# Kernel tuning notes

Measured on AMD Instinct MI355X. Metric: run time of the kernel, lower is better.

Reference implementation:

```python
import jax, jax.numpy as jnp
import numpy as np

N_QUBITS = 4
N_LAYERS = 2


def _ry(theta):
    # PennyLane RY(theta) = [[cos(t/2), -sin(t/2)], [sin(t/2), cos(t/2)]]
    c = jnp.cos(theta / 2)
    s = jnp.sin(theta / 2)
    return jnp.stack([jnp.stack([c, -s]), jnp.stack([s, c])]).astype(jnp.complex64)


def _rz(theta):
    # PennyLane RZ(theta) = diag(exp(-i t/2), exp(+i t/2))
    e = jnp.exp(-0.5j * theta.astype(jnp.complex64))
    return jnp.diag(jnp.stack([e, jnp.conj(e)]))


def _apply_1q(state, U, wire):
    # state: (2,)*N_QUBITS complex; contract U into axis `wire`
    state = jnp.tensordot(U, state, axes=((1,), (wire,)))
    return jnp.moveaxis(state, 0, wire)


def _cnot(state, ctrl, tgt):
    s = jnp.moveaxis(state, ctrl, 0)
    t2 = tgt - 1 if tgt > ctrl else tgt
    s1 = jnp.flip(s[1], axis=t2)  # X on target where control == 1
    return jnp.moveaxis(jnp.stack([s[0], s1]), 0, ctrl)


def _circuit(angles, weights):
    # angles: (N_QUBITS,), weights: (N_LAYERS, N_QUBITS, 2)
    state = jnp.zeros((2,) * N_QUBITS, jnp.complex64).at[(0,) * N_QUBITS].set(1.0)
    for i in range(N_QUBITS):
        state = _apply_1q(state, _ry(angles[i]), i)
    for l in range(N_LAYERS):
        for i in range(N_QUBITS):
            state = _apply_1q(state, _ry(weights[l, i, 0]), i)
            state = _apply_1q(state, _rz(weights[l, i, 1]), i)
        for i in range(N_QUBITS - 1):
            state = _cnot(state, i, i + 1)
        state = _cnot(state, N_QUBITS - 1, 0)
    probs = jnp.abs(state) ** 2
    p = probs.reshape(2, -1).sum(axis=1)  # marginal on wire 0
    return p[0] - p[1]  # <Z_0>


def setup_inputs() -> dict:
    key = jax.random.key(0)
    ks = jax.random.split(key, 6)
    B = 65536
    return {
        "x": jax.random.normal(ks[0], (B, 256), jnp.float32),
        "W1": jax.random.normal(ks[1], (64, 256), jnp.float32) * 0.0625,
        "b1": jax.random.normal(ks[2], (64,), jnp.float32) * 0.01,
        "W2": jax.random.normal(ks[3], (4, 64), jnp.float32) * 0.125,
        "b2": jax.random.normal(ks[4], (4,), jnp.float32) * 0.01,
        "q_weights": jax.random.normal(ks[5], (N_LAYERS, N_QUBITS, 2), jnp.float32) * 0.1,
    }


def reference(x, W1, b1, W2, b2, q_weights):
    h = jax.nn.relu(x @ W1.T + b1)          # [B, 64]
    angles = jnp.tanh(h @ W2.T + b2)         # [B, 4]
    z = jax.vmap(lambda a: _circuit(a, q_weights))(angles)  # [B]
    return z[:, None]                        # [B, 1]
```

## Files before the change

### kernel.cpp

```cpp
#include <hip/hip_runtime.h>
#include <math.h>

#define BM   64
#define BK   64
#define KDIM 256
#define LDSW 68
#define HSW  65

__global__ __launch_bounds__(256, 4)
void qc_fused(const float* __restrict__ x,
              const float* __restrict__ W1,
              const float* __restrict__ b1,
              const float* __restrict__ W2,
              const float* __restrict__ b2,
              const float* __restrict__ qw,
              float* __restrict__ out)
{
    __shared__ float smem[2 * BK * LDSW];
    __shared__ float w2s[4 * 64];
    __shared__ float b1s[64];
    __shared__ float b2s[4];
    __shared__ float trig[2 * 4 * 4];

    float (*xs)[LDSW] = (float(*)[LDSW])smem;
    float (*ws)[LDSW] = (float(*)[LDSW])(smem + BK * LDSW);

    const int tid  = threadIdx.x;
    const int tx   = tid & 15;
    const int ty   = tid >> 4;
    const int row0 = blockIdx.x * BM;

    w2s[tid] = W2[tid];
    if (tid < 64) b1s[tid] = b1[tid];
    if (tid < 4)  b2s[tid] = b2[tid];
    if (tid < 8) {
        int l = tid >> 2, i = tid & 3;
        float wy = qw[(l * 4 + i) * 2 + 0];
        float wz = qw[(l * 4 + i) * 2 + 1];
        float sy, cy, sz, cz;
        sincosf(0.5f * wy, &sy, &cy);
        sincosf(0.5f * wz, &sz, &cz);
        trig[(l * 4 + i) * 4 + 0] = cy;
        trig[(l * 4 + i) * 4 + 1] = sy;
        trig[(l * 4 + i) * 4 + 2] = cz;
        trig[(l * 4 + i) * 4 + 3] = sz;
    }

    float acc[4][4] = {};

    const int lr = tid >> 4;
    const int kq = tid & 15;

    for (int kt = 0; kt < KDIM / BK; ++kt) {
        if (kt) __syncthreads();
        #pragma unroll
        for (int rr = 0; rr < 4; ++rr) {
            int r = rr * 16 + lr;
            float4 xv = *(const float4*)(x  + (size_t)(row0 + r) * KDIM + kt * BK + kq * 4);
            float4 wv = *(const float4*)(W1 + (size_t)r          * KDIM + kt * BK + kq * 4);
            xs[kq * 4 + 0][r] = xv.x; xs[kq * 4 + 1][r] = xv.y;
            xs[kq * 4 + 2][r] = xv.z; xs[kq * 4 + 3][r] = xv.w;
            ws[kq * 4 + 0][r] = wv.x; ws[kq * 4 + 1][r] = wv.y;
            ws[kq * 4 + 2][r] = wv.z; ws[kq * 4 + 3][r] = wv.w;
        }
        __syncthreads();
        #pragma unroll 8
        for (int k = 0; k < BK; ++k) {
            float4 xa = *(const float4*)&xs[k][4 * ty];
            float4 wa = *(const float4*)&ws[k][4 * tx];
            float xr[4] = {xa.x, xa.y, xa.z, xa.w};
            float wc[4] = {wa.x, wa.y, wa.z, wa.w};
            #pragma unroll
            for (int i = 0; i < 4; ++i)
                #pragma unroll
                for (int j = 0; j < 4; ++j)
                    acc[i][j] = fmaf(xr[i], wc[j], acc[i][j]);
        }
    }
    __syncthreads();

    float* hsf = smem;
    #pragma unroll
    for (int i = 0; i < 4; ++i)
        #pragma unroll
        for (int j = 0; j < 4; ++j) {
            float v = acc[i][j] + b1s[4 * tx + j];
            hsf[(4 * ty + i) * HSW + (4 * tx + j)] = fmaxf(v, 0.0f);
        }
    __syncthreads();

    float* angs = smem + BK * LDSW;
    {
        int r = tid & 63, qi = tid >> 6;
        float s = b2s[qi];
        #pragma unroll 16
        for (int k = 0; k < 64; ++k)
            s = fmaf(hsf[r * HSW + k], w2s[qi * 64 + k], s);
        angs[r * 4 + qi] = tanhf(s);
    }
    __syncthreads();

    if (tid < 64) {
        float ca[4], sa[4];
        #pragma unroll
        for (int i = 0; i < 4; ++i) {
            float a = angs[tid * 4 + i];
            __sincosf(0.5f * a, &sa[i], &ca[i]);
        }
        float re[16], im[16];
        #pragma unroll
        for (int idx = 0; idx < 16; ++idx) {
            re[idx] = (idx & 8 ? sa[0] : ca[0]) * (idx & 4 ? sa[1] : ca[1]) *
                      (idx & 2 ? sa[2] : ca[2]) * (idx & 1 ? sa[3] : ca[3]);
            im[idx] = 0.0f;
        }
        #pragma unroll
        for (int l = 0; l < 2; ++l) {
            #pragma unroll
            for (int i = 0; i < 4; ++i) {
                const float cy = trig[(l * 4 + i) * 4 + 0];
                const float sy = trig[(l * 4 + i) * 4 + 1];
                const float cz = trig[(l * 4 + i) * 4 + 2];
                const float sz = trig[(l * 4 + i) * 4 + 3];
                const int m = 8 >> i;
                #pragma unroll
                for (int idx = 0; idx < 16; ++idx) {
                    if (!(idx & m)) {
                        int j = idx | m;
                        float ar = re[idx], ai = im[idx], br = re[j], bi = im[j];
                        re[idx] = fmaf(cy, ar, -sy * br);
                        im[idx] = fmaf(cy, ai, -sy * bi);
                        re[j]   = fmaf(sy, ar,  cy * br);
                        im[j]   = fmaf(sy, ai,  cy * bi);
                    }
                }
                #pragma unroll
                for (int idx = 0; idx < 16; ++idx) {
                    float sgn = (idx & m) ? sz : -sz;
                    float ar = re[idx], ai = im[idx];
                    re[idx] = fmaf(ar, cz, -ai * sgn);
                    im[idx] = fmaf(ar, sgn, ai * cz);
                }
            }
            #pragma unroll
            for (int c = 0; c < 4; ++c) {
                int t  = (c + 1) & 3;
                int mc = 8 >> c, mt = 8 >> t;
                #pragma unroll
                for (int idx = 0; idx < 16; ++idx) {
                    if ((idx & mc) && !(idx & mt)) {
                        int j = idx | mt;
                        float tr = re[idx]; re[idx] = re[j]; re[j] = tr;
                        float ti = im[idx]; im[idx] = im[j]; im[j] = ti;
                    }
                }
            }
        }
        float z = 0.0f;
        #pragma unroll
        for (int idx = 0; idx < 16; ++idx) {
            float p = re[idx] * re[idx] + im[idx] * im[idx];
            z += (idx & 8) ? -p : p;
        }
        out[row0 + tid] = z;
    }
}

extern "C" void kernel_launch(void* const* d_in, const int* in_sizes, int n_in,
                              void* d_out, int out_size, void* d_ws, size_t ws_size,
                              hipStream_t stream) {
    const float* x   = (const float*)d_in[0];
    const float* W1  = (const float*)d_in[1];
    const float* b1  = (const float*)d_in[2];
    const float* W2  = (const float*)d_in[3];
    const float* b2  = (const float*)d_in[4];
    const float* qw  = (const float*)d_in[5];
    float* out = (float*)d_out;
    const int B = in_sizes[0] / KDIM;
    qc_fused<<<B / BM, 256, 0, stream>>>(x, W1, b1, W2, b2, qw, out);
}
```

Baseline: 130.1 us.

## Use fp16 MFMA for first layer GEMM with larger row tiles

Replaces the scalar FP32 FMA GEMM for x@W1^T with MFMA 16x16x32 f16 instructions. Inputs are converted to half when staged into LDS. The block tile grows to 128 rows with a K chunk of 128, and occupancy is lowered to 2 blocks. The second layer and the quantum circuit are fused into one thread per row, which drops a sync and the shared angle buffer. Converting to fp16 loses input precision and may break tolerance. The workload is mostly memory-bound on reading x (64 MB), so the compute savings may be limited.

```diff
diff --git a/kernel.cpp b/kernel.cpp
--- a/kernel.cpp
+++ b/kernel.cpp
@@ -1,13 +1,17 @@
 #include <hip/hip_runtime.h>
 #include <math.h>
 
-#define BM   64
-#define BK   64
+typedef _Float16 half8  __attribute__((ext_vector_type(8)));
+typedef _Float16 half4v __attribute__((ext_vector_type(4)));
+typedef float    float4v __attribute__((ext_vector_type(4)));
+
+#define BM   128
 #define KDIM 256
-#define LDSW 68
+#define BKF  128
+#define XSTR 136
 #define HSW  65
 
-__global__ __launch_bounds__(256, 4)
+__global__ __launch_bounds__(256, 2)
 void qc_fused(const float* __restrict__ x,
               const float* __restrict__ W1,
               const float* __restrict__ b1,
@@ -16,18 +20,18 @@
               const float* __restrict__ qw,
               float* __restrict__ out)
 {
-    __shared__ float smem[2 * BK * LDSW];
-    __shared__ float w2s[4 * 64];
+    __shared__ _Float16 xh[BM * XSTR];
+    __shared__ _Float16 wh[64 * XSTR];
+    __shared__ float w2s[256];
     __shared__ float b1s[64];
     __shared__ float b2s[4];
-    __shared__ float trig[2 * 4 * 4];
-
-    float (*xs)[LDSW] = (float(*)[LDSW])smem;
-    float (*ws)[LDSW] = (float(*)[LDSW])(smem + BK * LDSW);
+    __shared__ float trig[32];
 
     const int tid  = threadIdx.x;
-    const int tx   = tid & 15;
-    const int ty   = tid >> 4;
+    const int lane = tid & 63;
+    const int wv   = tid >> 6;
+    const int m    = lane & 15;
+    const int q    = lane >> 4;
     const int row0 = blockIdx.x * BM;
 
     w2s[tid] = W2[tid];
@@ -46,67 +50,85 @@
         trig[(l * 4 + i) * 4 + 3] = sz;
     }
 
-    float acc[4][4] = {};
-
-    const int lr = tid >> 4;
-    const int kq = tid & 15;
-
-    for (int kt = 0; kt < KDIM / BK; ++kt) {
-        if (kt) __syncthreads();
-        #pragma unroll
-        for (int rr = 0; rr < 4; ++rr) {
-            int r = rr * 16 + lr;
-            float4 xv = *(const float4*)(x  + (size_t)(row0 + r) * KDIM + kt * BK + kq * 4);
-            float4 wv = *(const float4*)(W1 + (size_t)r          * KDIM + kt * BK + kq * 4);
-            xs[kq * 4 + 0][r] = xv.x; xs[kq * 4 + 1][r] = xv.y;
-            xs[kq * 4 + 2][r] = xv.z; xs[kq * 4 + 3][r] = xv.w;
-            ws[kq * 4 + 0][r] = wv.x; ws[kq * 4 + 1][r] = wv.y;
-            ws[kq * 4 + 2][r] = wv.z; ws[kq * 4 + 3][r] = wv.w;
+    float4v acc[2][4] = {};
+
+    const int sr  = tid >> 3, skq = tid & 7;
+    const int wr  = tid >> 2, wkq = tid & 3;
+
+    for (int kc = 0; kc < KDIM; kc += BKF) {
+        if (kc) __syncthreads();
+        #pragma unroll
+        for (int i = 0; i < 4; ++i) {
+            #pragma unroll
+            for (int j = 0; j < 4; ++j) {
+                int row = sr + 32 * i;
+                int kf  = 4 * skq + 32 * j;
+                const float4v v = *(const float4v*)(x + (size_t)(row0 + row) * KDIM + kc + kf);
+                half4v h;
+                h[0] = (_Float16)v[0]; h[1] = (_Float16)v[1];
+                h[2] = (_Float16)v[2]; h[3] = (_Float16)v[3];
+                *(half4v*)&xh[row * XSTR + kf] = h;
+            }
+        }
+        #pragma unroll
+        for (int j = 0; j < 8; ++j) {
+            int kf = 4 * wkq + 16 * j;
+            const float4v v = *(const float4v*)(W1 + (size_t)wr * KDIM + kc + kf);
+            half4v h;
+            h[0] = (_Float16)v[0]; h[1] = (_Float16)v[1];
+            h[2] = (_Float16)v[2]; h[3] = (_Float16)v[3];
+            *(half4v*)&wh[wr * XSTR + kf] = h;
         }
         __syncthreads();
+        #pragma unroll
+        for (int ks = 0; ks < 4; ++ks) {
+            const int ko = ks * 32 + q * 8;
+            half8 af0 = *(const half8*)&xh[(wv * 32 +      m) * XSTR + ko];
+            half8 af1 = *(const half8*)&xh[(wv * 32 + 16 + m) * XSTR + ko];
+            #pragma unroll
+            for (int b = 0; b < 4; ++b) {
+                half8 bf = *(const half8*)&wh[(16 * b + m) * XSTR + ko];
+                acc[0][b] = __builtin_amdgcn_mfma_f32_16x16x32_f16(af0, bf, acc[0][b], 0, 0, 0);
+                acc[1][b] = __builtin_amdgcn_mfma_f32_16x16x32_f16(af1, bf, acc[1][b], 0, 0, 0);
+            }
+        }
+    }
+    __syncthreads();
+
+    float* hs = (float*)xh;
+    #pragma unroll
+    for (int a = 0; a < 2; ++a) {
+        #pragma unroll
+        for (int b = 0; b < 4; ++b) {
+            #pragma unroll
+            for (int i = 0; i < 4; ++i) {
+                int row = wv * 32 + 16 * a + 4 * q + i;
+                int col = 16 * b + m;
+                float v = acc[a][b][i] + b1s[col];
+                hs[row * HSW + col] = fmaxf(v, 0.0f);
+            }
+        }
+    }
+    __syncthreads();
+
+    if (tid < BM) {
+        const int r = tid;
+        float s0 = b2s[0], s1 = b2s[1], s2 = b2s[2], s3 = b2s[3];
         #pragma unroll 8
-        for (int k = 0; k < BK; ++k) {
-            float4 xa = *(const float4*)&xs[k][4 * ty];
-            float4 wa = *(const float4*)&ws[k][4 * tx];
-            float xr[4] = {xa.x, xa.y, xa.z, xa.w};
-            float wc[4] = {wa.x, wa.y, wa.z, wa.w};
-            #pragma unroll
-            for (int i = 0; i < 4; ++i)
-                #pragma unroll
-                for (int j = 0; j < 4; ++j)
-                    acc[i][j] = fmaf(xr[i], wc[j], acc[i][j]);
-        }
-    }
-    __syncthreads();
-
-    float* hsf = smem;
-    #pragma unroll
-    for (int i = 0; i < 4; ++i)
-        #pragma unroll
-        for (int j = 0; j < 4; ++j) {
-            float v = acc[i][j] + b1s[4 * tx + j];
-            hsf[(4 * ty + i) * HSW + (4 * tx + j)] = fmaxf(v, 0.0f);
-        }
-    __syncthreads();
-
-    float* angs = smem + BK * LDSW;
-    {
-        int r = tid & 63, qi = tid >> 6;
-        float s = b2s[qi];
-        #pragma unroll 16
-        for (int k = 0; k < 64; ++k)
-            s = fmaf(hsf[r * HSW + k], w2s[qi * 64 + k], s);
-        angs[r * 4 + qi] = tanhf(s);
-    }
-    __syncthreads();
-
-    if (tid < 64) {
+        for (int k = 0; k < 64; ++k) {
+            float hv = hs[r * HSW + k];
+            s0 = fmaf(hv, w2s[0 * 64 + k], s0);
+            s1 = fmaf(hv, w2s[1 * 64 + k], s1);
+            s2 = fmaf(hv, w2s[2 * 64 + k], s2);
+            s3 = fmaf(hv, w2s[3 * 64 + k], s3);
+        }
+        float ang[4] = { tanhf(s0), tanhf(s1), tanhf(s2), tanhf(s3) };
+
         float ca[4], sa[4];
         #pragma unroll
-        for (int i = 0; i < 4; ++i) {
-            float a = angs[tid * 4 + i];
-            __sincosf(0.5f * a, &sa[i], &ca[i]);
-        }
+        for (int i = 0; i < 4; ++i)
+            __sincosf(0.5f * ang[i], &sa[i], &ca[i]);
+
         float re[16], im[16];
         #pragma unroll
         for (int idx = 0; idx < 16; ++idx) {
@@ -122,11 +144,11 @@
                 const float sy = trig[(l * 4 + i) * 4 + 1];
                 const float cz = trig[(l * 4 + i) * 4 + 2];
                 const float sz = trig[(l * 4 + i) * 4 + 3];
-                const int m = 8 >> i;
+                const int mq = 8 >> i;
                 #pragma unroll
                 for (int idx = 0; idx < 16; ++idx) {
-                    if (!(idx & m)) {
-                        int j = idx | m;
+                    if (!(idx & mq)) {
+                        int j = idx | mq;
                         float ar = re[idx], ai = im[idx], br = re[j], bi = im[j];
                         re[idx] = fmaf(cy, ar, -sy * br);
                         im[idx] = fmaf(cy, ai, -sy * bi);
@@ -136,7 +158,7 @@
                 }
                 #pragma unroll
                 for (int idx = 0; idx < 16; ++idx) {
-                    float sgn = (idx & m) ? sz : -sz;
+                    float sgn = (idx & mq) ? sz : -sz;
                     float ar = re[idx], ai = im[idx];
                     re[idx] = fmaf(ar, cz, -ai * sgn);
                     im[idx] = fmaf(ar, sgn, ai * cz);
@@ -162,19 +184,19 @@
             float p = re[idx] * re[idx] + im[idx] * im[idx];
             z += (idx & 8) ? -p : p;
         }
-        out[row0 + tid] = z;
+        out[row0 + r] = z;
     }
 }
 
 extern "C" void kernel_launch(void* const* d_in, const int* in_sizes, int n_in,
                               void* d_out, int out_size, void* d_ws, size_t ws_size,
                               hipStream_t stream) {
-    const float* x   = (const float*)d_in[0];
-    const float* W1  = (const float*)d_in[1];
-    const float* b1  = (const float*)d_in[2];
-    const float* W2  = (const float*)d_in[3];
-    const float* b2  = (const float*)d_in[4];
-    const float* qw  = (const float*)d_in[5];
+    const float* x  = (const float*)d_in[0];
+    const float* W1 = (const float*)d_in[1];
+    const float* b1 = (const float*)d_in[2];
+    const float* W2 = (const float*)d_in[3];
+    const float* b2 = (const float*)d_in[4];
+    const float* qw = (const float*)d_in[5];
     float* out = (float*)d_out;
     const int B = in_sizes[0] / KDIM;
     qc_fused<<<B / BM, 256, 0, stream>>>(x, W1, b1, W2, b2, qw, out);
```

Result: faster. 104.5 us (-19.7%).
